# Performance work log

Measured on AMD Instinct MI355X. Metric: run time of the kernel, lower is better.

Reference implementation:

```python
import jax, jax.numpy as jnp
import numpy as np

K_V_DIM = 100
_SQRT_D = float(np.sqrt(K_V_DIM))


def _dk_layer(q, k, v, Wq, bq, Wk, n_unsqueeze):
    """One DKEncoder_layer: DK_text + DK_knowledge + DK_fusion (CokeBert attention).
    q: [B, q_dim]; k: [..., n, K_V_DIM]; v: [..., n, d_v].
    Attention over the last neighbor axis n.
    """
    # DK_text: linear + tanh + unsqueeze to broadcast against k
    q_i = jnp.tanh(q @ Wq.T + bq)                               # [B, D]
    q_i = q_i.reshape((q_i.shape[0],) + (1,) * n_unsqueeze + (K_V_DIM,))
    # DK_knowledge: bias-free linear on k
    k = k @ Wk.T
    # DK_fusion (CokeBert): scaled dot, mask zeros, leaky_relu+softmax, zero out fully-masked rows
    attn = (q_i * k).sum(-1) / _SQRT_D                          # [..., n]
    attn = jnp.where(attn == 0.0, -10000.0, attn)
    attn = jax.nn.softmax(jax.nn.leaky_relu(attn), axis=-1)
    n = attn.shape[-1]
    attn = jnp.where(attn == 1.0 / n, 0.0, attn)
    return jnp.einsum('...n,...nd->...d', attn, v)              # [..., d_v]


def setup_inputs() -> dict:
    key = jax.random.key(0)
    ks = jax.random.split(key, 12)
    B, S, E, N1, N2, D, Q = 8, 256, 256, 16, 16, K_V_DIM, 768
    return {
        "input_ent": jax.random.randint(ks[0], (B, S), 0, 2, dtype=jnp.int64),
        "q": jax.random.normal(ks[1], (B, S, Q), dtype=jnp.float32),
        "k1": jax.random.normal(ks[2], (B, E, N1, D), dtype=jnp.float32),
        "v1": jax.random.normal(ks[3], (B, E, N1, D), dtype=jnp.float32),
        "k2": jax.random.normal(ks[4], (B, E, N1, N2, D), dtype=jnp.float32),
        "v2": jax.random.normal(ks[5], (B, E, N1, N2, D), dtype=jnp.float32),
        # layers[0] has layer_no=2 (deepest), layers[1] has layer_no=1
        "Wq2": jax.random.normal(ks[6], (D, Q), dtype=jnp.float32) * 0.05,
        "bq2": jnp.zeros((D,), dtype=jnp.float32),
        "Wk2": jax.random.normal(ks[7], (D, D), dtype=jnp.float32) * 0.1,
        "Wq1": jax.random.normal(ks[8], (D, Q), dtype=jnp.float32) * 0.05,
        "bq1": jnp.zeros((D,), dtype=jnp.float32),
        "Wk1": jax.random.normal(ks[9], (D, D), dtype=jnp.float32) * 0.1,
    }


def reference(input_ent, q, k1, v1, k2, v2, Wq2, bq2, Wk2, Wq1, bq1, Wk1):
    q0 = q[:, 0, :]                                             # [B, Q]
    # layer 0 (layer_no=2): reduce innermost neighbor axis
    combined = _dk_layer(q0, k2, v2, Wq2, bq2, Wk2, 3)          # [B, E, N1, D]
    # layer 1 (layer_no=1): v = cat([v1, combined])
    v1c = jnp.concatenate([v1, combined], axis=-1)              # [B, E, N1, 2D]
    combined = _dk_layer(q0, k1, v1c, Wq1, bq1, Wk1, 2)         # [B, E, 2D]
    # scatter: i-th nonzero position of input_ent[b] receives combined[b, i]
    mask = input_ent != 0                                       # [B, S]
    rank = jnp.cumsum(mask.astype(jnp.int32), axis=1) - 1       # [B, S]
    rank = jnp.clip(rank, 0, combined.shape[1] - 1)
    gathered = jnp.take_along_axis(combined, rank[..., None], axis=1)  # [B, S, 2D]
    return jnp.where(mask[..., None], gathered, 0.0)
```

## Files before the change

kernel.cpp:

```cpp
#include <hip/hip_runtime.h>
#include <cstddef>
#include <cstdint>

#define BB 8
#define SS 256
#define EE 256
#define NN1 16
#define NN2 16
#define DD 100
#define QQ 768

__global__ __launch_bounds__(256) void prep_kernel(
    const float* __restrict__ q, const int* __restrict__ ent,
    const float* __restrict__ Wq2, const float* __restrict__ bq2, const float* __restrict__ Wk2,
    const float* __restrict__ Wq1, const float* __restrict__ bq1, const float* __restrict__ Wk1,
    float* __restrict__ qk2o, float* __restrict__ qk1o, int* __restrict__ rk)
{
    const int blk = blockIdx.x, t = threadIdx.x;
    if (blk < 16) {
        const int b = blk >> 1, layer = blk & 1;
        const float* Wq = layer ? Wq1 : Wq2;
        const float* bq = layer ? bq1 : bq2;
        const float* Wk = layer ? Wk1 : Wk2;
        float* qko      = layer ? qk1o : qk2o;
        __shared__ float s_q[QQ];
        __shared__ float s_qi[DD];
        for (int i = t; i < QQ; i += 256) s_q[i] = q[(size_t)b * SS * QQ + i];
        __syncthreads();
        const int r = t & 7;
        for (int d = t >> 3; d < DD; d += 32) {
            float acc = 0.f;
            for (int i = r; i < QQ; i += 8) acc += Wq[(size_t)d * QQ + i] * s_q[i];
            acc += __shfl_xor(acc, 1, 8);
            acc += __shfl_xor(acc, 2, 8);
            acc += __shfl_xor(acc, 4, 8);
            if (r == 0) s_qi[d] = tanhf(acc + bq[d]);
        }
        __syncthreads();
        if (t < DD) {
            float acc = 0.f;
            for (int d = 0; d < DD; ++d) acc += s_qi[d] * Wk[d * DD + t];
            qko[b * DD + t] = 0.1f * acc;
        }
    } else {
        const int b = blk - 16;
        __shared__ int s_m[SS];
        const int m = (ent[b * SS + t] != 0) ? 1 : 0;
        s_m[t] = m;
        __syncthreads();
        for (int off = 1; off < SS; off <<= 1) {
            const int add = (t >= off) ? s_m[t - off] : 0;
            __syncthreads();
            s_m[t] += add;
            __syncthreads();
        }
        int rank = s_m[t] - 1;
        rank = rank < 0 ? 0 : (rank > EE - 1 ? EE - 1 : rank);
        rk[b * SS + t] = m ? rank : -1;
    }
}

__global__ __launch_bounds__(256) void main_kernel(
    const float* __restrict__ k1, const float* __restrict__ v1,
    const float* __restrict__ k2, const float* __restrict__ v2,
    const float* __restrict__ qk1g, const float* __restrict__ qk2g,
    float* __restrict__ comb)
{
    const int be = blockIdx.x;
    const int b  = be >> 8;
    const int t  = threadIdx.x;

    __shared__ float s_k[NN2 * DD];
    __shared__ float s_v[NN2 * DD];
    __shared__ float s_c2[NN1 * DD];
    __shared__ float s_qk[DD];
    __shared__ float s_logit[16];
    __shared__ float s_p[16];
    float4* sk4 = reinterpret_cast<float4*>(s_k);
    float4* sv4 = reinterpret_cast<float4*>(s_v);

    if (t < DD) s_qk[t] = qk2g[b * DD + t];

    const int gi = t >> 4;
    const int rr = t & 15;

    for (int n1 = 0; n1 < NN1; ++n1) {
        __syncthreads();
        const float4* gk = reinterpret_cast<const float4*>(k2 + (size_t)(be * NN1 + n1) * (NN2 * DD));
        const float4* gv = reinterpret_cast<const float4*>(v2 + (size_t)(be * NN1 + n1) * (NN2 * DD));
        for (int i = t; i < 400; i += 256) { sk4[i] = gk[i]; sv4[i] = gv[i]; }
        __syncthreads();

        float acc = 0.f;
        for (int d = rr; d < DD; d += 16) acc += s_k[gi * DD + d] * s_qk[d];
        acc += __shfl_xor(acc, 1, 16);
        acc += __shfl_xor(acc, 2, 16);
        acc += __shfl_xor(acc, 4, 16);
        acc += __shfl_xor(acc, 8, 16);
        if (rr == 0) {
            float lg = acc;
            if (lg == 0.0f) lg = -10000.0f;
            lg = lg >= 0.f ? lg : 0.01f * lg;
            s_logit[gi] = lg;
        }
        __syncthreads();
        if (t < 16) {
            const float lg = s_logit[t];
            float mx = lg;
            mx = fmaxf(mx, __shfl_xor(mx, 1, 16));
            mx = fmaxf(mx, __shfl_xor(mx, 2, 16));
            mx = fmaxf(mx, __shfl_xor(mx, 4, 16));
            mx = fmaxf(mx, __shfl_xor(mx, 8, 16));
            const float e = __expf(lg - mx);
            float sm = e;
            sm += __shfl_xor(sm, 1, 16);
            sm += __shfl_xor(sm, 2, 16);
            sm += __shfl_xor(sm, 4, 16);
            sm += __shfl_xor(sm, 8, 16);
            float p = e / sm;
            if (p == 0.0625f) p = 0.f;
            s_p[t] = p;
        }
        __syncthreads();
        if (t < DD) {
            float a2 = 0.f;
            #pragma unroll
            for (int n2 = 0; n2 < NN2; ++n2) a2 += s_p[n2] * s_v[n2 * DD + t];
            s_c2[n1 * DD + t] = a2;
        }
    }

    __syncthreads();
    if (t < DD) s_qk[t] = qk1g[b * DD + t];
    {
        const float4* gk = reinterpret_cast<const float4*>(k1 + (size_t)be * (NN1 * DD));
        const float4* gv = reinterpret_cast<const float4*>(v1 + (size_t)be * (NN1 * DD));
        for (int i = t; i < 400; i += 256) { sk4[i] = gk[i]; sv4[i] = gv[i]; }
    }
    __syncthreads();

    float acc = 0.f;
    for (int d = rr; d < DD; d += 16) acc += s_k[gi * DD + d] * s_qk[d];
    acc += __shfl_xor(acc, 1, 16);
    acc += __shfl_xor(acc, 2, 16);
    acc += __shfl_xor(acc, 4, 16);
    acc += __shfl_xor(acc, 8, 16);
    if (rr == 0) {
        float lg = acc;
        if (lg == 0.0f) lg = -10000.0f;
        lg = lg >= 0.f ? lg : 0.01f * lg;
        s_logit[gi] = lg;
    }
    __syncthreads();
    if (t < 16) {
        const float lg = s_logit[t];
        float mx = lg;
        mx = fmaxf(mx, __shfl_xor(mx, 1, 16));
        mx = fmaxf(mx, __shfl_xor(mx, 2, 16));
        mx = fmaxf(mx, __shfl_xor(mx, 4, 16));
        mx = fmaxf(mx, __shfl_xor(mx, 8, 16));
        const float e = __expf(lg - mx);
        float sm = e;
        sm += __shfl_xor(sm, 1, 16);
        sm += __shfl_xor(sm, 2, 16);
        sm += __shfl_xor(sm, 4, 16);
        sm += __shfl_xor(sm, 8, 16);
        float p = e / sm;
        if (p == 0.0625f) p = 0.f;
        s_p[t] = p;
    }
    __syncthreads();
    if (t < 2 * DD) {
        float a1 = 0.f;
        if (t < DD) {
            #pragma unroll
            for (int n1 = 0; n1 < NN1; ++n1) a1 += s_p[n1] * s_v[n1 * DD + t];
        } else {
            const int d = t - DD;
            #pragma unroll
            for (int n1 = 0; n1 < NN1; ++n1) a1 += s_p[n1] * s_c2[n1 * DD + d];
        }
        comb[(size_t)be * (2 * DD) + t] = a1;
    }
}

__global__ __launch_bounds__(64) void gather_kernel(
    const float* __restrict__ comb, const int* __restrict__ rk, float* __restrict__ out)
{
    const int bs = blockIdx.x;
    const int b  = bs >> 8;
    const int t  = threadIdx.x;
    const int r  = rk[bs];
    float* o = out + (size_t)bs * (2 * DD);
    if (r < 0) {
        for (int d = t; d < 2 * DD; d += 64) o[d] = 0.f;
    } else {
        const float* src = comb + (size_t)(b * EE + r) * (2 * DD);
        for (int d = t; d < 2 * DD; d += 64) o[d] = src[d];
    }
}

extern "C" void kernel_launch(void* const* d_in, const int* in_sizes, int n_in,
                              void* d_out, int out_size, void* d_ws, size_t ws_size,
                              hipStream_t stream)
{
    const int*   ent = (const int*)d_in[0];
    const float* q   = (const float*)d_in[1];
    const float* k1  = (const float*)d_in[2];
    const float* v1  = (const float*)d_in[3];
    const float* k2  = (const float*)d_in[4];
    const float* v2  = (const float*)d_in[5];
    const float* Wq2 = (const float*)d_in[6];
    const float* bq2 = (const float*)d_in[7];
    const float* Wk2 = (const float*)d_in[8];
    const float* Wq1 = (const float*)d_in[9];
    const float* bq1 = (const float*)d_in[10];
    const float* Wk1 = (const float*)d_in[11];
    float* out = (float*)d_out;

    float* ws   = (float*)d_ws;
    float* qk2  = ws;
    float* qk1  = ws + 1024;
    float* comb = ws + 4096;
    int*   rk   = (int*)(ws + 4096 + 409600);

    prep_kernel<<<24, 256, 0, stream>>>(q, ent, Wq2, bq2, Wk2, Wq1, bq1, Wk1, qk2, qk1, rk);
    main_kernel<<<BB * EE, 256, 0, stream>>>(k1, v1, k2, v2, qk1, qk2, comb);
    gather_kernel<<<BB * SS, 64, 0, stream>>>(comb, rk, out);
}
```

Baseline: 161.6 us.

## Register-prefetch next K/V tile, pad shared K rows, compute softmax redundantly per wave

The main kernel now loads the next n1 slice of k2/v2 (and finally k1/v1) into registers while the current slice is being processed, so global load latency overlaps compute. Shared K rows are padded to 104 floats to reduce bank conflicts in the dot-product reads. Each wave now computes the softmax redundantly and broadcasts the probabilities through shuffles instead of shared memory, which removes a barrier per iteration. The cost is higher register pressure from the prefetch buffers and extra redundant shuffle work.

```diff
diff --git a/kernel.cpp b/kernel.cpp
--- a/kernel.cpp
+++ b/kernel.cpp
@@ -70,29 +70,53 @@
     const int b  = be >> 8;
     const int t  = threadIdx.x;
 
-    __shared__ float s_k[NN2 * DD];
+    __shared__ float s_k[NN2 * 104];
     __shared__ float s_v[NN2 * DD];
     __shared__ float s_c2[NN1 * DD];
-    __shared__ float s_qk[DD];
+    __shared__ float s_qk2[DD];
+    __shared__ float s_qk1[DD];
     __shared__ float s_logit[16];
-    __shared__ float s_p[16];
     float4* sk4 = reinterpret_cast<float4*>(s_k);
     float4* sv4 = reinterpret_cast<float4*>(s_v);
 
-    if (t < DD) s_qk[t] = qk2g[b * DD + t];
+    if (t < DD) { s_qk2[t] = qk2g[b * DD + t]; s_qk1[t] = qk1g[b * DD + t]; }
 
     const int gi = t >> 4;
     const int rr = t & 15;
-
-    for (int n1 = 0; n1 < NN1; ++n1) {
-        __syncthreads();
-        const float4* gk = reinterpret_cast<const float4*>(k2 + (size_t)(be * NN1 + n1) * (NN2 * DD));
-        const float4* gv = reinterpret_cast<const float4*>(v2 + (size_t)(be * NN1 + n1) * (NN2 * DD));
-        for (int i = t; i < 400; i += 256) { sk4[i] = gk[i]; sv4[i] = gv[i]; }
-        __syncthreads();
-
+    const int i1 = t + 256;
+
+    const int ks0 = (t  / 25) * 26 + (t  % 25);
+    const int ks1 = (i1 / 25) * 26 + (i1 % 25);
+
+    float4 rk0, rk1, rv0, rv1;
+    {
+        const float4* gk = reinterpret_cast<const float4*>(k2 + (size_t)be * NN1 * (NN2 * DD));
+        const float4* gv = reinterpret_cast<const float4*>(v2 + (size_t)be * NN1 * (NN2 * DD));
+        rk0 = gk[t]; rv0 = gv[t];
+        if (t < 144) { rk1 = gk[i1]; rv1 = gv[i1]; }
+    }
+
+    for (int it = 0; it <= NN1; ++it) {
+        __syncthreads();
+        sk4[ks0] = rk0;
+        sv4[t]   = rv0;
+        if (t < 144) { sk4[ks1] = rk1; sv4[i1] = rv1; }
+        __syncthreads();
+
+        if (it < NN1) {
+            const float* kb = (it < NN1 - 1) ? k2 + ((size_t)(be * NN1 + it + 1)) * (NN2 * DD)
+                                             : k1 + (size_t)be * (NN1 * DD);
+            const float* vb = (it < NN1 - 1) ? v2 + ((size_t)(be * NN1 + it + 1)) * (NN2 * DD)
+                                             : v1 + (size_t)be * (NN1 * DD);
+            const float4* gk = reinterpret_cast<const float4*>(kb);
+            const float4* gv = reinterpret_cast<const float4*>(vb);
+            rk0 = gk[t]; rv0 = gv[t];
+            if (t < 144) { rk1 = gk[i1]; rv1 = gv[i1]; }
+        }
+
+        const float* qk = (it == NN1) ? s_qk1 : s_qk2;
         float acc = 0.f;
-        for (int d = rr; d < DD; d += 16) acc += s_k[gi * DD + d] * s_qk[d];
+        for (int d = rr; d < DD; d += 16) acc += s_k[gi * 104 + d] * qk[d];
         acc += __shfl_xor(acc, 1, 16);
         acc += __shfl_xor(acc, 2, 16);
         acc += __shfl_xor(acc, 4, 16);
@@ -100,66 +124,17 @@
         if (rr == 0) {
             float lg = acc;
             if (lg == 0.0f) lg = -10000.0f;
-            lg = lg >= 0.f ? lg : 0.01f * lg;
-            s_logit[gi] = lg;
-        }
-        __syncthreads();
-        if (t < 16) {
-            const float lg = s_logit[t];
-            float mx = lg;
-            mx = fmaxf(mx, __shfl_xor(mx, 1, 16));
-            mx = fmaxf(mx, __shfl_xor(mx, 2, 16));
-            mx = fmaxf(mx, __shfl_xor(mx, 4, 16));
-            mx = fmaxf(mx, __shfl_xor(mx, 8, 16));
-            const float e = __expf(lg - mx);
-            float sm = e;
-            sm += __shfl_xor(sm, 1, 16);
-            sm += __shfl_xor(sm, 2, 16);
-            sm += __shfl_xor(sm, 4, 16);
-            sm += __shfl_xor(sm, 8, 16);
-            float p = e / sm;
-            if (p == 0.0625f) p = 0.f;
-            s_p[t] = p;
-        }
-        __syncthreads();
-        if (t < DD) {
-            float a2 = 0.f;
-            #pragma unroll
-            for (int n2 = 0; n2 < NN2; ++n2) a2 += s_p[n2] * s_v[n2 * DD + t];
-            s_c2[n1 * DD + t] = a2;
-        }
-    }
-
-    __syncthreads();
-    if (t < DD) s_qk[t] = qk1g[b * DD + t];
-    {
-        const float4* gk = reinterpret_cast<const float4*>(k1 + (size_t)be * (NN1 * DD));
-        const float4* gv = reinterpret_cast<const float4*>(v1 + (size_t)be * (NN1 * DD));
-        for (int i = t; i < 400; i += 256) { sk4[i] = gk[i]; sv4[i] = gv[i]; }
-    }
-    __syncthreads();
-
-    float acc = 0.f;
-    for (int d = rr; d < DD; d += 16) acc += s_k[gi * DD + d] * s_qk[d];
-    acc += __shfl_xor(acc, 1, 16);
-    acc += __shfl_xor(acc, 2, 16);
-    acc += __shfl_xor(acc, 4, 16);
-    acc += __shfl_xor(acc, 8, 16);
-    if (rr == 0) {
-        float lg = acc;
-        if (lg == 0.0f) lg = -10000.0f;
-        lg = lg >= 0.f ? lg : 0.01f * lg;
-        s_logit[gi] = lg;
-    }
-    __syncthreads();
-    if (t < 16) {
-        const float lg = s_logit[t];
+            s_logit[gi] = lg >= 0.f ? lg : 0.01f * lg;
+        }
+        __syncthreads();
+
+        float lg = s_logit[t & 15];
         float mx = lg;
         mx = fmaxf(mx, __shfl_xor(mx, 1, 16));
         mx = fmaxf(mx, __shfl_xor(mx, 2, 16));
         mx = fmaxf(mx, __shfl_xor(mx, 4, 16));
         mx = fmaxf(mx, __shfl_xor(mx, 8, 16));
-        const float e = __expf(lg - mx);
+        float e = __expf(lg - mx);
         float sm = e;
         sm += __shfl_xor(sm, 1, 16);
         sm += __shfl_xor(sm, 2, 16);
@@ -167,20 +142,30 @@
         sm += __shfl_xor(sm, 8, 16);
         float p = e / sm;
         if (p == 0.0625f) p = 0.f;
-        s_p[t] = p;
-    }
-    __syncthreads();
-    if (t < 2 * DD) {
-        float a1 = 0.f;
-        if (t < DD) {
-            #pragma unroll
-            for (int n1 = 0; n1 < NN1; ++n1) a1 += s_p[n1] * s_v[n1 * DD + t];
+        float pn[16];
+        #pragma unroll
+        for (int n = 0; n < 16; ++n) pn[n] = __shfl(p, n, 64);
+
+        if (it < NN1) {
+            if (t < DD) {
+                float a = 0.f;
+                #pragma unroll
+                for (int n = 0; n < 16; ++n) a += pn[n] * s_v[n * DD + t];
+                s_c2[it * DD + t] = a;
+            }
         } else {
-            const int d = t - DD;
-            #pragma unroll
-            for (int n1 = 0; n1 < NN1; ++n1) a1 += s_p[n1] * s_c2[n1 * DD + d];
-        }
-        comb[(size_t)be * (2 * DD) + t] = a1;
+            if (t < 2 * DD) {
+                float a = 0.f;
+                if (t < DD) {
+                    #pragma unroll
+                    for (int n = 0; n < 16; ++n) a += pn[n] * s_v[n * DD + t];
+                } else {
+                    #pragma unroll
+                    for (int n = 0; n < 16; ++n) a += pn[n] * s_c2[n * DD + (t - DD)];
+                }
+                comb[(size_t)be * (2 * DD) + t] = a;
+            }
+        }
     }
 }
 
```

Measured after the change: 173.9 us. +7.6%, slower.

## Split fused two-level attention into per-n1 blocks plus a second-level kernel

Applied to the files above, without the earlier changes.

The single main kernel, which ran a serial loop over 16 first-level neighbors per block, is replaced by two kernels. dk2_kernel launches one block per (b,e,n1), reads k2 and v2 directly from global memory without shared staging, and writes intermediate c2 to workspace. dk1_kernel then runs the outer attention using c2, with batches chunked to fit the workspace. This gives more parallelism and fewer barriers per block, at the cost of an extra round trip through global memory for c2 and extra launches when the workspace is small.

```diff
diff --git a/kernel.cpp b/kernel.cpp
--- a/kernel.cpp
+++ b/kernel.cpp
@@ -60,87 +60,31 @@
     }
 }
 
-__global__ __launch_bounds__(256) void main_kernel(
-    const float* __restrict__ k1, const float* __restrict__ v1,
+__global__ __launch_bounds__(256) void dk2_kernel(
     const float* __restrict__ k2, const float* __restrict__ v2,
-    const float* __restrict__ qk1g, const float* __restrict__ qk2g,
-    float* __restrict__ comb)
-{
-    const int be = blockIdx.x;
-    const int b  = be >> 8;
-    const int t  = threadIdx.x;
-
-    __shared__ float s_k[NN2 * DD];
-    __shared__ float s_v[NN2 * DD];
-    __shared__ float s_c2[NN1 * DD];
-    __shared__ float s_qk[DD];
+    const float* __restrict__ qk2g, float* __restrict__ c2, int b0)
+{
+    const int blk = blockIdx.x;
+    const int n1  = blk & 15;
+    const int bbe = blk >> 4;
+    const int b   = b0 + (bbe >> 8);
+    const int t   = threadIdx.x;
+    const int gi  = t >> 4;
+    const int rr  = t & 15;
+
     __shared__ float s_logit[16];
     __shared__ float s_p[16];
-    float4* sk4 = reinterpret_cast<float4*>(s_k);
-    float4* sv4 = reinterpret_cast<float4*>(s_v);
-
-    if (t < DD) s_qk[t] = qk2g[b * DD + t];
-
-    const int gi = t >> 4;
-    const int rr = t & 15;
-
-    for (int n1 = 0; n1 < NN1; ++n1) {
-        __syncthreads();
-        const float4* gk = reinterpret_cast<const float4*>(k2 + (size_t)(be * NN1 + n1) * (NN2 * DD));
-        const float4* gv = reinterpret_cast<const float4*>(v2 + (size_t)(be * NN1 + n1) * (NN2 * DD));
-        for (int i = t; i < 400; i += 256) { sk4[i] = gk[i]; sv4[i] = gv[i]; }
-        __syncthreads();
-
-        float acc = 0.f;
-        for (int d = rr; d < DD; d += 16) acc += s_k[gi * DD + d] * s_qk[d];
-        acc += __shfl_xor(acc, 1, 16);
-        acc += __shfl_xor(acc, 2, 16);
-        acc += __shfl_xor(acc, 4, 16);
-        acc += __shfl_xor(acc, 8, 16);
-        if (rr == 0) {
-            float lg = acc;
-            if (lg == 0.0f) lg = -10000.0f;
-            lg = lg >= 0.f ? lg : 0.01f * lg;
-            s_logit[gi] = lg;
-        }
-        __syncthreads();
-        if (t < 16) {
-            const float lg = s_logit[t];
-            float mx = lg;
-            mx = fmaxf(mx, __shfl_xor(mx, 1, 16));
-            mx = fmaxf(mx, __shfl_xor(mx, 2, 16));
-            mx = fmaxf(mx, __shfl_xor(mx, 4, 16));
-            mx = fmaxf(mx, __shfl_xor(mx, 8, 16));
-            const float e = __expf(lg - mx);
-            float sm = e;
-            sm += __shfl_xor(sm, 1, 16);
-            sm += __shfl_xor(sm, 2, 16);
-            sm += __shfl_xor(sm, 4, 16);
-            sm += __shfl_xor(sm, 8, 16);
-            float p = e / sm;
-            if (p == 0.0625f) p = 0.f;
-            s_p[t] = p;
-        }
-        __syncthreads();
-        if (t < DD) {
-            float a2 = 0.f;
-            #pragma unroll
-            for (int n2 = 0; n2 < NN2; ++n2) a2 += s_p[n2] * s_v[n2 * DD + t];
-            s_c2[n1 * DD + t] = a2;
-        }
-    }
-
-    __syncthreads();
-    if (t < DD) s_qk[t] = qk1g[b * DD + t];
-    {
-        const float4* gk = reinterpret_cast<const float4*>(k1 + (size_t)be * (NN1 * DD));
-        const float4* gv = reinterpret_cast<const float4*>(v1 + (size_t)be * (NN1 * DD));
-        for (int i = t; i < 400; i += 256) { sk4[i] = gk[i]; sv4[i] = gv[i]; }
-    }
-    __syncthreads();
-
+
+    const size_t base = ((size_t)(((b << 8) | (bbe & 255)) * 16 + n1)) * (size_t)(NN2 * DD);
+
+    const float* krow = k2 + base + gi * DD;
+    const float* qk   = qk2g + b * DD;
     float acc = 0.f;
-    for (int d = rr; d < DD; d += 16) acc += s_k[gi * DD + d] * s_qk[d];
+    #pragma unroll
+    for (int j = 0; j < 7; ++j) {
+        const int d = rr + 16 * j;
+        if (d < DD) acc += krow[d] * qk[d];
+    }
     acc += __shfl_xor(acc, 1, 16);
     acc += __shfl_xor(acc, 2, 16);
     acc += __shfl_xor(acc, 4, 16);
@@ -148,39 +92,102 @@
     if (rr == 0) {
         float lg = acc;
         if (lg == 0.0f) lg = -10000.0f;
-        lg = lg >= 0.f ? lg : 0.01f * lg;
-        s_logit[gi] = lg;
-    }
-    __syncthreads();
-    if (t < 16) {
-        const float lg = s_logit[t];
-        float mx = lg;
-        mx = fmaxf(mx, __shfl_xor(mx, 1, 16));
-        mx = fmaxf(mx, __shfl_xor(mx, 2, 16));
-        mx = fmaxf(mx, __shfl_xor(mx, 4, 16));
-        mx = fmaxf(mx, __shfl_xor(mx, 8, 16));
-        const float e = __expf(lg - mx);
-        float sm = e;
-        sm += __shfl_xor(sm, 1, 16);
-        sm += __shfl_xor(sm, 2, 16);
-        sm += __shfl_xor(sm, 4, 16);
-        sm += __shfl_xor(sm, 8, 16);
-        float p = e / sm;
-        if (p == 0.0625f) p = 0.f;
-        s_p[t] = p;
-    }
-    __syncthreads();
+        s_logit[gi] = lg >= 0.f ? lg : 0.01f * lg;
+    }
+    __syncthreads();
+
+    float lg = s_logit[t & 15];
+    float mx = lg;
+    mx = fmaxf(mx, __shfl_xor(mx, 1, 16));
+    mx = fmaxf(mx, __shfl_xor(mx, 2, 16));
+    mx = fmaxf(mx, __shfl_xor(mx, 4, 16));
+    mx = fmaxf(mx, __shfl_xor(mx, 8, 16));
+    const float e = __expf(lg - mx);
+    float sm = e;
+    sm += __shfl_xor(sm, 1, 16);
+    sm += __shfl_xor(sm, 2, 16);
+    sm += __shfl_xor(sm, 4, 16);
+    sm += __shfl_xor(sm, 8, 16);
+    float p = e / sm;
+    if (p == 0.0625f) p = 0.f;
+    if (t < 16) s_p[t] = p;
+    __syncthreads();
+
+    if (t < DD) {
+        const float* vb = v2 + base;
+        float a = 0.f;
+        #pragma unroll
+        for (int n = 0; n < NN2; ++n) a += s_p[n] * vb[n * DD + t];
+        c2[((size_t)bbe * NN1 + n1) * DD + t] = a;
+    }
+}
+
+__global__ __launch_bounds__(256) void dk1_kernel(
+    const float* __restrict__ k1, const float* __restrict__ v1,
+    const float* __restrict__ c2, const float* __restrict__ qk1g,
+    float* __restrict__ comb, int b0)
+{
+    const int bbe = blockIdx.x;
+    const int b   = b0 + (bbe >> 8);
+    const int be  = (b << 8) | (bbe & 255);
+    const int t   = threadIdx.x;
+    const int gi  = t >> 4;
+    const int rr  = t & 15;
+
+    __shared__ float s_logit[16];
+    __shared__ float s_p[16];
+
+    const size_t base = (size_t)be * (NN1 * DD);
+
+    const float* krow = k1 + base + gi * DD;
+    const float* qk   = qk1g + b * DD;
+    float acc = 0.f;
+    #pragma unroll
+    for (int j = 0; j < 7; ++j) {
+        const int d = rr + 16 * j;
+        if (d < DD) acc += krow[d] * qk[d];
+    }
+    acc += __shfl_xor(acc, 1, 16);
+    acc += __shfl_xor(acc, 2, 16);
+    acc += __shfl_xor(acc, 4, 16);
+    acc += __shfl_xor(acc, 8, 16);
+    if (rr == 0) {
+        float lg = acc;
+        if (lg == 0.0f) lg = -10000.0f;
+        s_logit[gi] = lg >= 0.f ? lg : 0.01f * lg;
+    }
+    __syncthreads();
+
+    float lg = s_logit[t & 15];
+    float mx = lg;
+    mx = fmaxf(mx, __shfl_xor(mx, 1, 16));
+    mx = fmaxf(mx, __shfl_xor(mx, 2, 16));
+    mx = fmaxf(mx, __shfl_xor(mx, 4, 16));
+    mx = fmaxf(mx, __shfl_xor(mx, 8, 16));
+    const float e = __expf(lg - mx);
+    float sm = e;
+    sm += __shfl_xor(sm, 1, 16);
+    sm += __shfl_xor(sm, 2, 16);
+    sm += __shfl_xor(sm, 4, 16);
+    sm += __shfl_xor(sm, 8, 16);
+    float p = e / sm;
+    if (p == 0.0625f) p = 0.f;
+    if (t < 16) s_p[t] = p;
+    __syncthreads();
+
     if (t < 2 * DD) {
-        float a1 = 0.f;
+        float a = 0.f;
         if (t < DD) {
+            const float* vb = v1 + base;
             #pragma unroll
-            for (int n1 = 0; n1 < NN1; ++n1) a1 += s_p[n1] * s_v[n1 * DD + t];
+            for (int n = 0; n < NN1; ++n) a += s_p[n] * vb[n * DD + t];
         } else {
             const int d = t - DD;
+            const float* cb = c2 + (size_t)bbe * (NN1 * DD);
             #pragma unroll
-            for (int n1 = 0; n1 < NN1; ++n1) a1 += s_p[n1] * s_c2[n1 * DD + d];
-        }
-        comb[(size_t)be * (2 * DD) + t] = a1;
+            for (int n = 0; n < NN1; ++n) a += s_p[n] * cb[n * DD + d];
+        }
+        comb[(size_t)be * (2 * DD) + t] = a;
     }
 }
 
@@ -221,10 +228,22 @@
     float* ws   = (float*)d_ws;
     float* qk2  = ws;
     float* qk1  = ws + 1024;
+    int*   rk   = (int*)(ws + 2048);
     float* comb = ws + 4096;
-    int*   rk   = (int*)(ws + 4096 + 409600);
+    float* c2   = ws + 4096 + 409600;
+
+    const size_t fixed = 4096 + 409600;
+    const size_t perb  = (size_t)EE * NN1 * DD;
+    size_t wsf = ws_size / sizeof(float);
+    int kb = (wsf > fixed) ? (int)((wsf - fixed) / perb) : 1;
+    if (kb < 1) kb = 1;
+    if (kb > BB) kb = BB;
 
     prep_kernel<<<24, 256, 0, stream>>>(q, ent, Wq2, bq2, Wk2, Wq1, bq1, Wk1, qk2, qk1, rk);
-    main_kernel<<<BB * EE, 256, 0, stream>>>(k1, v1, k2, v2, qk1, qk2, comb);
+    for (int b0 = 0; b0 < BB; b0 += kb) {
+        const int nb = (BB - b0 < kb) ? (BB - b0) : kb;
+        dk2_kernel<<<nb * EE * NN1, 256, 0, stream>>>(k2, v2, qk2, c2, b0);
+        dk1_kernel<<<nb * EE,       256, 0, stream>>>(k1, v1, c2, qk1, comb, b0);
+    }
     gather_kernel<<<BB * SS, 64, 0, stream>>>(comb, rk, out);
 }
```

Result: no change. 159.7 us (-1.1%).

## Split fused attention kernel into persistent layer-2 and layer-1 kernels with register prefetch

Applied to the files above, without the earlier changes.

Replaces the 256-thread block per (b,e) kernel, which looped serially over 16 N1 tiles with many barriers, with a persistent 64-thread dk2 kernel. Each block handles one (b,e,n1) unit at a time, keeps k/v tiles in registers and prefetches the next unit's k tile. The layer-2 results go to a workspace buffer that a separate dk1 kernel consumes, split into two halves per entity. The prep GEMV is also vectorised with float4. The changes add an intermediate global round trip of about 13 MB and a batching loop that depends on the workspace size.

```diff
diff --git a/kernel.cpp b/kernel.cpp
--- a/kernel.cpp
+++ b/kernel.cpp
@@ -9,6 +9,10 @@
 #define NN2 16
 #define DD 100
 #define QQ 768
+
+__device__ __forceinline__ float dot4(float4 a, float4 b) {
+    return a.x * b.x + a.y * b.y + a.z * b.z + a.w * b.w;
+}
 
 __global__ __launch_bounds__(256) void prep_kernel(
     const float* __restrict__ q, const int* __restrict__ ent,
@@ -27,10 +31,12 @@
         __shared__ float s_qi[DD];
         for (int i = t; i < QQ; i += 256) s_q[i] = q[(size_t)b * SS * QQ + i];
         __syncthreads();
+        const float4* sq4 = (const float4*)s_q;
         const int r = t & 7;
         for (int d = t >> 3; d < DD; d += 32) {
+            const float4* wq4 = (const float4*)(Wq + (size_t)d * QQ);
             float acc = 0.f;
-            for (int i = r; i < QQ; i += 8) acc += Wq[(size_t)d * QQ + i] * s_q[i];
+            for (int c = r; c < QQ / 4; c += 8) acc += dot4(wq4[c], sq4[c]);
             acc += __shfl_xor(acc, 1, 8);
             acc += __shfl_xor(acc, 2, 8);
             acc += __shfl_xor(acc, 4, 8);
@@ -60,52 +66,62 @@
     }
 }
 
-__global__ __launch_bounds__(256) void main_kernel(
-    const float* __restrict__ k1, const float* __restrict__ v1,
+__global__ __launch_bounds__(64) void dk2_kernel(
     const float* __restrict__ k2, const float* __restrict__ v2,
-    const float* __restrict__ qk1g, const float* __restrict__ qk2g,
-    float* __restrict__ comb)
-{
-    const int be = blockIdx.x;
-    const int b  = be >> 8;
-    const int t  = threadIdx.x;
-
-    __shared__ float s_k[NN2 * DD];
-    __shared__ float s_v[NN2 * DD];
-    __shared__ float s_c2[NN1 * DD];
-    __shared__ float s_qk[DD];
-    __shared__ float s_logit[16];
-    __shared__ float s_p[16];
-    float4* sk4 = reinterpret_cast<float4*>(s_k);
-    float4* sv4 = reinterpret_cast<float4*>(s_v);
-
-    if (t < DD) s_qk[t] = qk2g[b * DD + t];
-
-    const int gi = t >> 4;
-    const int rr = t & 15;
-
-    for (int n1 = 0; n1 < NN1; ++n1) {
-        __syncthreads();
-        const float4* gk = reinterpret_cast<const float4*>(k2 + (size_t)(be * NN1 + n1) * (NN2 * DD));
-        const float4* gv = reinterpret_cast<const float4*>(v2 + (size_t)(be * NN1 + n1) * (NN2 * DD));
-        for (int i = t; i < 400; i += 256) { sk4[i] = gk[i]; sv4[i] = gv[i]; }
-        __syncthreads();
-
-        float acc = 0.f;
-        for (int d = rr; d < DD; d += 16) acc += s_k[gi * DD + d] * s_qk[d];
-        acc += __shfl_xor(acc, 1, 16);
-        acc += __shfl_xor(acc, 2, 16);
-        acc += __shfl_xor(acc, 4, 16);
-        acc += __shfl_xor(acc, 8, 16);
-        if (rr == 0) {
-            float lg = acc;
-            if (lg == 0.0f) lg = -10000.0f;
-            lg = lg >= 0.f ? lg : 0.01f * lg;
-            s_logit[gi] = lg;
-        }
-        __syncthreads();
-        if (t < 16) {
-            const float lg = s_logit[t];
+    const float* __restrict__ qk2g, float* __restrict__ c2o,
+    int b0, int nunits)
+{
+    const int t = threadIdx.x;
+    __shared__ float4 s_pp[400];
+    float* s_part = (float*)s_pp;
+
+    int u = blockIdx.x;
+    const int stride = gridDim.x;
+    const size_t gofs = (size_t)b0 * 4096;
+
+    float4 ka[7];
+    if (u < nunits) {
+        const float4* kt = (const float4*)k2 + (gofs + u) * 400;
+        #pragma unroll
+        for (int j = 0; j < 6; ++j) ka[j] = kt[t + 64 * j];
+        if (t < 16) ka[6] = kt[384 + t];
+    }
+
+    while (u < nunits) {
+        const int b = b0 + (u >> 12);
+        const float4* qk = (const float4*)qk2g + b * 25;
+        const float4* vt = (const float4*)v2 + (gofs + u) * 400;
+
+        float4 va[7];
+        #pragma unroll
+        for (int j = 0; j < 6; ++j) va[j] = vt[t + 64 * j];
+        if (t < 16) va[6] = vt[384 + t];
+
+        #pragma unroll
+        for (int j = 0; j < 6; ++j) {
+            const int i = t + 64 * j;
+            s_part[i] = dot4(ka[j], qk[i % 25]);
+        }
+        if (t < 16) { const int i = 384 + t; s_part[i] = dot4(ka[6], qk[i % 25]); }
+
+        const int un = u + stride;
+        if (un < nunits) {
+            const float4* ktn = (const float4*)k2 + (gofs + un) * 400;
+            #pragma unroll
+            for (int j = 0; j < 6; ++j) ka[j] = ktn[t + 64 * j];
+            if (t < 16) ka[6] = ktn[384 + t];
+        }
+
+        __syncthreads();
+        float p = 0.f;
+        {
+            float lg = 0.f;
+            if (t < 16) {
+                #pragma unroll
+                for (int c = 0; c < 25; ++c) lg += s_part[t * 25 + c];
+                if (lg == 0.0f) lg = -10000.0f;
+                lg = lg >= 0.f ? lg : 0.01f * lg;
+            }
             float mx = lg;
             mx = fmaxf(mx, __shfl_xor(mx, 1, 16));
             mx = fmaxf(mx, __shfl_xor(mx, 2, 16));
@@ -117,43 +133,80 @@
             sm += __shfl_xor(sm, 2, 16);
             sm += __shfl_xor(sm, 4, 16);
             sm += __shfl_xor(sm, 8, 16);
-            float p = e / sm;
+            p = e / sm;
             if (p == 0.0625f) p = 0.f;
-            s_p[t] = p;
-        }
-        __syncthreads();
-        if (t < DD) {
-            float a2 = 0.f;
+        }
+        __syncthreads();
+
+        #pragma unroll
+        for (int j = 0; j < 6; ++j) {
+            const int i = t + 64 * j;
+            const float pn = __shfl(p, i / 25, 64);
+            s_pp[i] = make_float4(pn * va[j].x, pn * va[j].y, pn * va[j].z, pn * va[j].w);
+        }
+        if (t < 16) {
+            const int i = 384 + t;
+            const float pn = __shfl(p, 15, 64);
+            s_pp[i] = make_float4(pn * va[6].x, pn * va[6].y, pn * va[6].z, pn * va[6].w);
+        }
+        __syncthreads();
+
+        if (t < 25) {
+            float4 a = make_float4(0.f, 0.f, 0.f, 0.f);
             #pragma unroll
-            for (int n2 = 0; n2 < NN2; ++n2) a2 += s_p[n2] * s_v[n2 * DD + t];
-            s_c2[n1 * DD + t] = a2;
-        }
-    }
-
+            for (int n = 0; n < 16; ++n) {
+                const float4 x = s_pp[n * 25 + t];
+                a.x += x.x; a.y += x.y; a.z += x.z; a.w += x.w;
+            }
+            ((float4*)c2o)[(size_t)u * 25 + t] = a;
+        }
+        __syncthreads();
+        u = un;
+    }
+}
+
+__global__ __launch_bounds__(64) void dk1_kernel(
+    const float* __restrict__ k1, const float* __restrict__ v1,
+    const float* __restrict__ c2i, const float* __restrict__ qk1g,
+    float* __restrict__ comb, int b0)
+{
+    const int blk  = blockIdx.x;
+    const int bbe  = blk >> 1;
+    const int half = blk & 1;
+    const int b    = b0 + (bbe >> 8);
+    const int be   = (b << 8) | (bbe & 255);
+    const int t    = threadIdx.x;
+
+    __shared__ float4 s_pp[400];
+    float* s_part = (float*)s_pp;
+
+    const float4* kt = (const float4*)k1 + (size_t)be * 400;
+    const float4* vt = half ? (const float4*)c2i + (size_t)bbe * 400
+                            : (const float4*)v1 + (size_t)be * 400;
+    const float4* qk = (const float4*)qk1g + b * 25;
+
+    float4 ka[7], va[7];
+    #pragma unroll
+    for (int j = 0; j < 6; ++j) { ka[j] = kt[t + 64 * j]; va[j] = vt[t + 64 * j]; }
+    if (t < 16) { ka[6] = kt[384 + t]; va[6] = vt[384 + t]; }
+
+    #pragma unroll
+    for (int j = 0; j < 6; ++j) {
+        const int i = t + 64 * j;
+        s_part[i] = dot4(ka[j], qk[i % 25]);
+    }
+    if (t < 16) { const int i = 384 + t; s_part[i] = dot4(ka[6], qk[i % 25]); }
     __syncthreads();
-    if (t < DD) s_qk[t] = qk1g[b * DD + t];
+
+    float p = 0.f;
     {
-        const float4* gk = reinterpret_cast<const float4*>(k1 + (size_t)be * (NN1 * DD));
-        const float4* gv = reinterpret_cast<const float4*>(v1 + (size_t)be * (NN1 * DD));
-        for (int i = t; i < 400; i += 256) { sk4[i] = gk[i]; sv4[i] = gv[i]; }
-    }
-    __syncthreads();
-
-    float acc = 0.f;
-    for (int d = rr; d < DD; d += 16) acc += s_k[gi * DD + d] * s_qk[d];
-    acc += __shfl_xor(acc, 1, 16);
-    acc += __shfl_xor(acc, 2, 16);
-    acc += __shfl_xor(acc, 4, 16);
-    acc += __shfl_xor(acc, 8, 16);
-    if (rr == 0) {
-        float lg = acc;
-        if (lg == 0.0f) lg = -10000.0f;
-        lg = lg >= 0.f ? lg : 0.01f * lg;
-        s_logit[gi] = lg;
-    }
-    __syncthreads();
-    if (t < 16) {
-        const float lg = s_logit[t];
+        float lg = 0.f;
+        if (t < 16) {
+            #pragma unroll
+            for (int c = 0; c < 25; ++c) lg += s_part[t * 25 + c];
+            if (lg == 0.0f) lg = -10000.0f;
+            lg = lg >= 0.f ? lg : 0.01f * lg;
+        }
         float mx = lg;
         mx = fmaxf(mx, __shfl_xor(mx, 1, 16));
         mx = fmaxf(mx, __shfl_xor(mx, 2, 16));
@@ -165,22 +218,32 @@
         sm += __shfl_xor(sm, 2, 16);
         sm += __shfl_xor(sm, 4, 16);
         sm += __shfl_xor(sm, 8, 16);
-        float p = e / sm;
+        p = e / sm;
         if (p == 0.0625f) p = 0.f;
-        s_p[t] = p;
     }
     __syncthreads();
-    if (t < 2 * DD) {
-        float a1 = 0.f;
-        if (t < DD) {
-            #pragma unroll
-            for (int n1 = 0; n1 < NN1; ++n1) a1 += s_p[n1] * s_v[n1 * DD + t];
-        } else {
-            const int d = t - DD;
-            #pragma unroll
-            for (int n1 = 0; n1 < NN1; ++n1) a1 += s_p[n1] * s_c2[n1 * DD + d];
-        }
-        comb[(size_t)be * (2 * DD) + t] = a1;
+
+    #pragma unroll
+    for (int j = 0; j < 6; ++j) {
+        const int i = t + 64 * j;
+        const float pn = __shfl(p, i / 25, 64);
+        s_pp[i] = make_float4(pn * va[j].x, pn * va[j].y, pn * va[j].z, pn * va[j].w);
+    }
+    if (t < 16) {
+        const int i = 384 + t;
+        const float pn = __shfl(p, 15, 64);
+        s_pp[i] = make_float4(pn * va[6].x, pn * va[6].y, pn * va[6].z, pn * va[6].w);
+    }
+    __syncthreads();
+
+    if (t < 25) {
+        float4 a = make_float4(0.f, 0.f, 0.f, 0.f);
+        #pragma unroll
+        for (int n = 0; n < 16; ++n) {
+            const float4 x = s_pp[n * 25 + t];
+            a.x += x.x; a.y += x.y; a.z += x.z; a.w += x.w;
+        }
+        ((float4*)comb)[(size_t)be * 50 + half * 25 + t] = a;
     }
 }
 
@@ -221,10 +284,24 @@
     float* ws   = (float*)d_ws;
     float* qk2  = ws;
     float* qk1  = ws + 1024;
+    int*   rk   = (int*)(ws + 2048);
     float* comb = ws + 4096;
-    int*   rk   = (int*)(ws + 4096 + 409600);
+    float* c2   = ws + 4096 + 409600;
+
+    const size_t fixed = 4096 + 409600;
+    const size_t perb  = (size_t)EE * NN1 * DD;
+    size_t wsf = ws_size / sizeof(float);
+    int kb = (wsf > fixed) ? (int)((wsf - fixed) / perb) : 1;
+    if (kb < 1) kb = 1;
+    if (kb > BB) kb = BB;
 
     prep_kernel<<<24, 256, 0, stream>>>(q, ent, Wq2, bq2, Wk2, Wq1, bq1, Wk1, qk2, qk1, rk);
-    main_kernel<<<BB * EE, 256, 0, stream>>>(k1, v1, k2, v2, qk1, qk2, comb);
+    for (int b0 = 0; b0 < BB; b0 += kb) {
+        const int nb = (BB - b0 < kb) ? (BB - b0) : kb;
+        const int nunits = nb * EE * NN1;
+        const int grid = nunits < 4096 ? nunits : 4096;
+        dk2_kernel<<<grid, 64, 0, stream>>>(k2, v2, qk2, c2, b0, nunits);
+        dk1_kernel<<<nb * EE * 2, 64, 0, stream>>>(k1, v1, c2, qk1, comb, b0);
+    }
     gather_kernel<<<BB * SS, 64, 0, stream>>>(comb, rk, out);
 }
```

Result: faster. 155.0 us (-4.1%).
